# Kernel tuning notes

Measured on AMD Instinct MI355X. Metric: run time of the kernel, lower is better.

## Reference

```python
import jax, jax.numpy as jnp
import numpy as np

DIM = 768
HEADS = 12
HEAD_DIM = DIM // HEADS
EPS = 1e-6
LN_EPS = 1e-5


def setup_inputs() -> dict:
    key = jax.random.key(0)
    k1, k2, k3, k4 = jax.random.split(key, 4)
    x = jax.random.normal(k1, (8, 4096, DIM), dtype=jnp.float32)
    ln_gamma = jnp.ones((DIM,), dtype=jnp.float32)
    ln_beta = jnp.zeros((DIM,), dtype=jnp.float32)
    # torch nn.Linear weight layout: [out_features, in_features]
    w_qkv = jax.random.normal(k2, (3 * DIM, DIM), dtype=jnp.float32) * (1.0 / np.sqrt(DIM))
    w_proj = jax.random.normal(k3, (DIM, DIM), dtype=jnp.float32) * (1.0 / np.sqrt(DIM))
    b_proj = jax.random.normal(k4, (DIM,), dtype=jnp.float32) * 0.01
    return {"x": x, "ln_gamma": ln_gamma, "ln_beta": ln_beta,
            "w_qkv": w_qkv, "w_proj": w_proj, "b_proj": b_proj}


def _elu1(t):
    return jax.nn.elu(t) + 1.0


def reference(x, ln_gamma, ln_beta, w_qkv, w_proj, b_proj):
    bsz, n, dim = x.shape
    # LayerNorm
    mu = jnp.mean(x, axis=-1, keepdims=True)
    var = jnp.mean(jnp.square(x - mu), axis=-1, keepdims=True)
    y = (x - mu) * jax.lax.rsqrt(var + LN_EPS) * ln_gamma + ln_beta
    # qkv projection: [b, n, 3*dim]
    qkv = jnp.einsum('bnd,ed->bne', y, w_qkv)
    qkv = qkv.reshape(bsz, n, 3, HEADS, HEAD_DIM)
    qkv = jnp.transpose(qkv, (2, 0, 3, 1, 4))  # [3, b, h, n, hd]
    q, k, v = _elu1(qkv[0]), _elu1(qkv[1]), qkv[2]
    # kv outer-product sum over tokens: [b, h, d, e]
    kv = jnp.einsum('bhnd,bhne->bhde', k, v)
    k_sum = jnp.sum(k, axis=2)                              # [b, h, d]
    z = 1.0 / (jnp.einsum('bhnd,bhd->bhn', q, k_sum) + EPS)  # [b, h, n]
    out = jnp.einsum('bhnd,bhde->bhne', q, kv) * z[..., None]
    out = jnp.transpose(out, (0, 2, 1, 3)).reshape(bsz, n, dim)
    return jnp.einsum('bnd,ed->bne', out, w_proj) + b_proj
```

## Files before the change

### kernel.cpp

```cpp
#include <hip/hip_runtime.h>
#include <stdint.h>

typedef __bf16 bf16;
typedef __bf16 bf16x4 __attribute__((ext_vector_type(4)));
typedef __bf16 bf16x8 __attribute__((ext_vector_type(8)));
typedef float  f32x4  __attribute__((ext_vector_type(4)));

#define DIM   768
#define HEADS 12
#define HD    64
#define SEQ   4096
#define NKT2  12

__device__ __forceinline__ void gload16(const void* g, void* l) {
  typedef const __attribute__((address_space(1))) uint32_t* gp_t;
  typedef __attribute__((address_space(3))) uint32_t* lp_t;
  gp_t gp = reinterpret_cast<gp_t>(reinterpret_cast<uintptr_t>(g));
  lp_t lp = reinterpret_cast<lp_t>(reinterpret_cast<uintptr_t>(l));
  __builtin_amdgcn_global_load_lds(gp, lp, 16, 0, 0);
}

__global__ __launch_bounds__(256) void wcvt_kernel(const float* __restrict__ src,
                                                   bf16* __restrict__ dst) {
  int i = (blockIdx.x * 256 + threadIdx.x) * 4;
  float4 v = *reinterpret_cast<const float4*>(src + i);
  bf16x4 o;
  o[0] = (bf16)v.x; o[1] = (bf16)v.y; o[2] = (bf16)v.z; o[3] = (bf16)v.w;
  *reinterpret_cast<bf16x4*>(dst + i) = o;
}

__global__ __launch_bounds__(256) void ln_kernel(const float* __restrict__ x,
    const float* __restrict__ gam, const float* __restrict__ bet,
    bf16* __restrict__ y) {
  const int tid = threadIdx.x, w = tid >> 6, l = tid & 63;
  const int row = blockIdx.x * 4 + w;
  const float* xr = x + (long)row * DIM;
  float4 v[3];
  float s = 0.f, ss = 0.f;
#pragma unroll
  for (int j = 0; j < 3; j++) {
    v[j] = *reinterpret_cast<const float4*>(xr + l * 4 + j * 256);
    s  += v[j].x + v[j].y + v[j].z + v[j].w;
    ss += v[j].x * v[j].x + v[j].y * v[j].y + v[j].z * v[j].z + v[j].w * v[j].w;
  }
#pragma unroll
  for (int m = 1; m < 64; m <<= 1) { s += __shfl_xor(s, m); ss += __shfl_xor(ss, m); }
  const float mu = s * (1.f / 768.f);
  const float rstd = rsqrtf(ss * (1.f / 768.f) - mu * mu + 1e-5f);
  bf16* yr = y + (long)row * DIM;
#pragma unroll
  for (int j = 0; j < 3; j++) {
    int c = l * 4 + j * 256;
    float4 g4 = *reinterpret_cast<const float4*>(gam + c);
    float4 b4 = *reinterpret_cast<const float4*>(bet + c);
    bf16x4 o;
    o[0] = (bf16)((v[j].x - mu) * rstd * g4.x + b4.x);
    o[1] = (bf16)((v[j].y - mu) * rstd * g4.y + b4.y);
    o[2] = (bf16)((v[j].z - mu) * rstd * g4.z + b4.z);
    o[3] = (bf16)((v[j].w - mu) * rstd * g4.w + b4.w);
    *reinterpret_cast<bf16x4*>(yr + c) = o;
  }
}

template <int MODE>
__global__ __launch_bounds__(512, 4) void gemm_kernel(
    const bf16* __restrict__ A, const bf16* __restrict__ Bw,
    bf16* __restrict__ qb, bf16* __restrict__ kb, bf16* __restrict__ vb,
    float* __restrict__ outp, const float* __restrict__ bias) {
  __shared__ __align__(16) char lds[32768];
  const int tid = threadIdx.x;
  const int wid = tid >> 6, l = tid & 63;
  const int wr = wid >> 2, wc = wid & 3;
  const int l16 = l & 15, l4 = l >> 4;

  const int NT = (MODE == 0) ? 18 : 6;
  const int nwg = NT * 256;
  const int orig = blockIdx.x;
  const int wgid = (orig & 7) * (nwg >> 3) + (orig >> 3);
  const int mt = wgid / NT, nt = wgid % NT;

  const int L0 = tid * 16, L1 = 8192 + tid * 16;
  const int r0 = L0 >> 7, s0 = (L0 >> 4) & 7;
  const int r1 = L1 >> 7, s1 = (L1 >> 4) & 7;
  const bf16* pA0 = A + (long)(mt * 128 + r0) * DIM + (s0 ^ (r0 & 7)) * 8;
  const bf16* pA1 = A + (long)(mt * 128 + r1) * DIM + (s1 ^ (r1 & 7)) * 8;
  const bf16* pB0 = Bw + (long)(nt * 128 + r0) * DIM + (s0 ^ (r0 & 7)) * 8;
  const bf16* pB1 = Bw + (long)(nt * 128 + r1) * DIM + (s1 ^ (r1 & 7)) * 8;

  int offA[2][4], offB[2][2];
#pragma unroll
  for (int ks = 0; ks < 2; ks++) {
#pragma unroll
    for (int mi = 0; mi < 4; mi++) {
      int row = wr * 64 + mi * 16 + l16;
      offA[ks][mi] = row * 128 + (((l4 + 4 * ks) ^ (l16 & 7)) << 4);
    }
#pragma unroll
    for (int ni = 0; ni < 2; ni++) {
      int row = wc * 32 + ni * 16 + l16;
      offB[ks][ni] = 16384 + row * 128 + (((l4 + 4 * ks) ^ (l16 & 7)) << 4);
    }
  }

  f32x4 acc[4][2];
#pragma unroll
  for (int m = 0; m < 4; m++)
#pragma unroll
    for (int n = 0; n < 2; n++) { f32x4 z4 = {0.f, 0.f, 0.f, 0.f}; acc[m][n] = z4; }

  for (int t = 0; t < NKT2; t++) {
    __syncthreads();
    gload16(pA0 + t * 64, lds + L0);
    gload16(pA1 + t * 64, lds + L1);
    gload16(pB0 + t * 64, lds + 16384 + L0);
    gload16(pB1 + t * 64, lds + 16384 + L1);
    __syncthreads();
#pragma unroll
    for (int ks = 0; ks < 2; ks++) {
      bf16x8 a[4], b[2];
#pragma unroll
      for (int mi = 0; mi < 4; mi++)
        a[mi] = *reinterpret_cast<const bf16x8*>(lds + offA[ks][mi]);
#pragma unroll
      for (int ni = 0; ni < 2; ni++)
        b[ni] = *reinterpret_cast<const bf16x8*>(lds + offB[ks][ni]);
#pragma unroll
      for (int mi = 0; mi < 4; mi++)
#pragma unroll
        for (int ni = 0; ni < 2; ni++)
          acc[mi][ni] = __builtin_amdgcn_mfma_f32_16x16x32_bf16(a[mi], b[ni], acc[mi][ni], 0, 0, 0);
    }
  }

  if constexpr (MODE == 0) {
    const int s = nt / 6;
    const int j = nt % 6;
    if (s == 0) {
      bf16* Cs = (bf16*)lds;
      __syncthreads();
#pragma unroll
      for (int mi = 0; mi < 4; mi++)
#pragma unroll
        for (int ni = 0; ni < 2; ni++)
#pragma unroll
          for (int i = 0; i < 4; i++) {
            float val = acc[mi][ni][i];
            val = val > 0.f ? val + 1.f : __expf(val);
            Cs[(wr * 64 + mi * 16 + l4 * 4 + i) * 128 + wc * 32 + ni * 16 + l16] = (bf16)val;
          }
      __syncthreads();
#pragma unroll
      for (int it = 0; it < 4; it++) {
        int bi = it * 8192 + tid * 16;
        int row = bi >> 8;
        int col = (bi & 255) >> 1;
        int h = j * 2 + (col >> 6), d = col & 63;
        int trow = mt * 128 + row;
        int bb = trow >> 12, tok = trow & 4095;
        *reinterpret_cast<bf16x8*>(qb +
            ((long)(bb * HEADS + h) * SEQ + tok) * HD + d) =
            *reinterpret_cast<const bf16x8*>(Cs + (bi >> 1));
      }
    } else {
      bf16* dst0 = (s == 1) ? kb : vb;
      __syncthreads();
#pragma unroll
      for (int mi = 0; mi < 4; mi++)
#pragma unroll
        for (int ni = 0; ni < 2; ni++)
#pragma unroll
          for (int i = 0; i < 4; i++) {
            float val = acc[mi][ni][i];
            if (s == 1) val = val > 0.f ? val + 1.f : __expf(val);
            int tr = wr * 64 + mi * 16 + l4 * 4 + i;
            int cc = wc * 32 + ni * 16 + l16;
            *reinterpret_cast<bf16*>(lds + tr * 256 + ((cc * 2) ^ ((tr & 7) << 4))) = (bf16)val;
          }
      __syncthreads();
      const int cc = tid & 127;
      const int sp2 = tid >> 7;
      const int hh = j * 2 + (cc >> 6), dd = cc & 63;
      const int bb = (mt * 128) >> 12;
      const int n0 = ((mt * 128) & 4095) + sp2 * 32;
      bf16* dstp = dst0 + ((long)(bb * HEADS + hh) * HD + dd) * SEQ + n0;
#pragma unroll
      for (int q8i = 0; q8i < 4; q8i++) {
        bf16x8 o;
#pragma unroll
        for (int jj = 0; jj < 8; jj++) {
          int tok = sp2 * 32 + q8i * 8 + jj;
          o[jj] = *reinterpret_cast<const bf16*>(lds + tok * 256 + ((cc * 2) ^ ((tok & 7) << 4)));
        }
        *reinterpret_cast<bf16x8*>(dstp + q8i * 8) = o;
      }
    }
  } else {
#pragma unroll
    for (int ni = 0; ni < 2; ni++) {
      int col = nt * 128 + wc * 32 + ni * 16 + l16;
      float bv = bias[col];
#pragma unroll
      for (int mi = 0; mi < 4; mi++)
#pragma unroll
        for (int i = 0; i < 4; i++) {
          long trow = mt * 128 + wr * 64 + mi * 16 + l4 * 4 + i;
          outp[trow * DIM + col] = acc[mi][ni][i] + bv;
        }
    }
  }
}

__global__ __launch_bounds__(256) void kv_kernel(
    const bf16* __restrict__ ktb, const bf16* __restrict__ vtb,
    float* __restrict__ kv_part, float* __restrict__ ks_part) {
  __shared__ __align__(16) char lds[32768];
  const int head = blockIdx.x, sp = blockIdx.y;
  const int tid = threadIdx.x;
  const int wid = tid >> 6, l = tid & 63;
  const int wd = wid >> 1, we = wid & 1;
  const int l16 = l & 15, l4 = l >> 4;

  int offK[4][2], offV[4][2];
#pragma unroll
  for (int ks = 0; ks < 4; ks++) {
#pragma unroll
    for (int mi = 0; mi < 2; mi++) {
      int row = wd * 32 + mi * 16 + l16;
      offK[ks][mi] = row * 256 + ((ks * 64 + l4 * 16) ^ ((row & 7) << 4));
    }
#pragma unroll
    for (int ni = 0; ni < 2; ni++) {
      int row = we * 32 + ni * 16 + l16;
      offV[ks][ni] = 16384 + row * 256 + ((ks * 64 + l4 * 16) ^ ((row & 7) << 4));
    }
  }
  const bf16* srcK[4]; const bf16* srcV[4]; int ldst[4];
#pragma unroll
  for (int g = 0; g < 4; g++) {
    int L = g * 4096 + tid * 16;
    int r = L >> 8, cb = L & 255;
    int ce = (cb ^ ((r & 7) << 4)) >> 1;
    srcK[g] = ktb + ((long)head * HD + r) * SEQ + sp * 512 + ce;
    srcV[g] = vtb + ((long)head * HD + r) * SEQ + sp * 512 + ce;
    ldst[g] = L;
  }

  f32x4 acc[2][2];
#pragma unroll
  for (int m = 0; m < 2; m++)
#pragma unroll
    for (int n = 0; n < 2; n++) { f32x4 z4 = {0.f, 0.f, 0.f, 0.f}; acc[m][n] = z4; }
  float ksf = 0.f;
  const int ksd = tid >> 2, ksq = tid & 3;

  for (int c = 0; c < 4; c++) {
    __syncthreads();
#pragma unroll
    for (int g = 0; g < 4; g++) {
      gload16(srcK[g] + c * 128, lds + ldst[g]);
      gload16(srcV[g] + c * 128, lds + 16384 + ldst[g]);
    }
    __syncthreads();
#pragma unroll
    for (int q = 0; q < 4; q++) {
      bf16x8 k8 = *reinterpret_cast<const bf16x8*>(
          lds + ksd * 256 + ((ksq * 64 + q * 16) ^ ((ksd & 7) << 4)));
#pragma unroll
      for (int jj = 0; jj < 8; jj++) ksf += (float)k8[jj];
    }
#pragma unroll
    for (int ks = 0; ks < 4; ks++) {
      bf16x8 a[2], b[2];
      a[0] = *reinterpret_cast<const bf16x8*>(lds + offK[ks][0]);
      a[1] = *reinterpret_cast<const bf16x8*>(lds + offK[ks][1]);
      b[0] = *reinterpret_cast<const bf16x8*>(lds + offV[ks][0]);
      b[1] = *reinterpret_cast<const bf16x8*>(lds + offV[ks][1]);
#pragma unroll
      for (int mi = 0; mi < 2; mi++)
#pragma unroll
        for (int ni = 0; ni < 2; ni++)
          acc[mi][ni] = __builtin_amdgcn_mfma_f32_16x16x32_bf16(a[mi], b[ni], acc[mi][ni], 0, 0, 0);
    }
  }
  ksf += __shfl_xor(ksf, 1);
  ksf += __shfl_xor(ksf, 2);
  if (ksq == 0) ks_part[(head * 8 + sp) * 64 + ksd] = ksf;

  __syncthreads();
#pragma unroll
  for (int mi = 0; mi < 2; mi++)
#pragma unroll
    for (int ni = 0; ni < 2; ni++)
#pragma unroll
      for (int i = 0; i < 4; i++) {
        int dd = wd * 32 + mi * 16 + l4 * 4 + i;
        int ee = we * 32 + ni * 16 + l16;
        *reinterpret_cast<float*>(lds + dd * 256 + ((ee * 4) ^ ((dd & 7) << 4))) = acc[mi][ni][i];
      }
  __syncthreads();
  float* dst = kv_part + (long)(head * 8 + sp) * 4096;
  const int dd2 = tid >> 2, eq = tid & 3;
#pragma unroll
  for (int q = 0; q < 4; q++) {
    f32x4 v4 = *reinterpret_cast<const f32x4*>(
        lds + dd2 * 256 + ((eq * 64 + q * 16) ^ ((dd2 & 7) << 4)));
    *reinterpret_cast<f32x4*>(dst + dd2 * 64 + eq * 16 + q * 4) = v4;
  }
}

__global__ __launch_bounds__(256) void kvfin_kernel(const float* __restrict__ kv_part,
    const float* __restrict__ ks_part, bf16* __restrict__ kvT, float* __restrict__ ksum) {
  const int head = blockIdx.x, tid = threadIdx.x;
  const long base = (long)head * 8 * 4096;
  const int d = tid >> 2, ecol = (tid & 3) * 16;
  float s[16];
#pragma unroll
  for (int q = 0; q < 16; q++) s[q] = 0.f;
  for (int sp = 0; sp < 8; sp++) {
    const float* p = kv_part + base + sp * 4096 + d * 64 + ecol;
#pragma unroll
    for (int q = 0; q < 16; q++) s[q] += p[q];
  }
#pragma unroll
  for (int q = 0; q < 16; q++) kvT[head * 4096 + (ecol + q) * 64 + d] = (bf16)s[q];
  if (tid < 64) {
    float t = 0.f;
    for (int sp = 0; sp < 8; sp++) t += ks_part[(head * 8 + sp) * 64 + tid];
    ksum[head * 64 + tid] = t;
  }
}

__global__ __launch_bounds__(256) void qout_kernel(const bf16* __restrict__ qb,
    const bf16* __restrict__ kvT, const float* __restrict__ ksum,
    bf16* __restrict__ outp) {
  __shared__ __align__(16) bf16 Qs[128 * 64];
  __shared__ __align__(16) bf16 Bs2[64 * 64];
  __shared__ float ksum_s[64];
  __shared__ float z_s[128];
  const int head = blockIdx.x, tt = blockIdx.y;
  const int b = head / HEADS, h = head % HEADS;
  const int tid = threadIdx.x, w = tid >> 6, l = tid & 63;
  const int l16 = l & 15, l4 = l >> 4;
  const bf16* Qg = qb + (long)(head * SEQ + tt * 128) * HD;
#pragma unroll
  for (int r = 0; r < 4; r++) gload16(Qg + r * 2048 + tid * 8, Qs + r * 2048 + tid * 8);
#pragma unroll
  for (int r = 0; r < 2; r++)
    gload16(kvT + head * 4096 + r * 2048 + tid * 8, Bs2 + r * 2048 + tid * 8);
  if (tid < 64) ksum_s[tid] = ksum[head * 64 + tid];
  __syncthreads();
  {
    const int tok = tid >> 1, hf = tid & 1;
    float dsum = 0.f;
#pragma unroll
    for (int q = 0; q < 4; q++) {
      bf16x8 q8 = *reinterpret_cast<const bf16x8*>(Qs + tok * 64 + hf * 32 + q * 8);
#pragma unroll
      for (int jj = 0; jj < 8; jj++) dsum += (float)q8[jj] * ksum_s[hf * 32 + q * 8 + jj];
    }
    dsum += __shfl_xor(dsum, 1);
    if (hf == 0) z_s[tok] = 1.f / (dsum + 1e-6f);
  }
  f32x4 acc[2][4];
#pragma unroll
  for (int m = 0; m < 2; m++)
#pragma unroll
    for (int n = 0; n < 4; n++) { f32x4 z4 = {0.f, 0.f, 0.f, 0.f}; acc[m][n] = z4; }
#pragma unroll
  for (int kk = 0; kk < 2; kk++) {
    bf16x8 af[2], bfr[4];
#pragma unroll
    for (int m = 0; m < 2; m++)
      af[m] = *reinterpret_cast<const bf16x8*>(Qs + (w * 32 + m * 16 + l16) * 64 + kk * 32 + l4 * 8);
#pragma unroll
    for (int n = 0; n < 4; n++)
      bfr[n] = *reinterpret_cast<const bf16x8*>(Bs2 + (n * 16 + l16) * 64 + kk * 32 + l4 * 8);
#pragma unroll
    for (int m = 0; m < 2; m++)
#pragma unroll
      for (int n = 0; n < 4; n++)
        acc[m][n] = __builtin_amdgcn_mfma_f32_16x16x32_bf16(af[m], bfr[n], acc[m][n], 0, 0, 0);
  }
  __syncthreads();
#pragma unroll
  for (int m = 0; m < 2; m++)
#pragma unroll
    for (int n = 0; n < 4; n++)
#pragma unroll
      for (int i = 0; i < 4; i++) {
        int row = w * 32 + m * 16 + l4 * 4 + i;
        Qs[row * 64 + n * 16 + l16] = (bf16)(acc[m][n][i] * z_s[row]);
      }
  __syncthreads();
#pragma unroll
  for (int r = 0; r < 4; r++) {
    int idx = r * 2048 + tid * 8;
    int row = idx >> 6, col = idx & 63;
    *reinterpret_cast<bf16x8*>(outp + (long)(b * SEQ + tt * 128 + row) * DIM + h * HD + col) =
        *reinterpret_cast<const bf16x8*>(Qs + idx);
  }
}

extern "C" void kernel_launch(void* const* d_in, const int* in_sizes, int n_in,
                              void* d_out, int out_size, void* d_ws, size_t ws_size,
                              hipStream_t stream) {
  const float* x     = (const float*)d_in[0];
  const float* gam   = (const float*)d_in[1];
  const float* bet   = (const float*)d_in[2];
  const float* wqkv  = (const float*)d_in[3];
  const float* wproj = (const float*)d_in[4];
  const float* bproj = (const float*)d_in[5];
  float* out = (float*)d_out;
  char* ws = (char*)d_ws;

  bf16*  y       = (bf16*)(ws);
  bf16*  qb      = (bf16*)(ws + 50331648);
  bf16*  kb      = (bf16*)(ws + 100663296);
  bf16*  vb      = (bf16*)(ws + 150994944);
  bf16*  wqkv_b  = (bf16*)(ws + 201326592);
  bf16*  wproj_b = (bf16*)(ws + 204865536);
  float* kv_part = (float*)(ws + 206045184);
  float* ks_part = (float*)(ws + 218628096);
  bf16*  kvT     = (bf16*)(ws + 218824704);
  float* ksum    = (float*)(ws + 219611136);

  wcvt_kernel<<<1728, 256, 0, stream>>>(wqkv, wqkv_b);
  wcvt_kernel<<<576, 256, 0, stream>>>(wproj, wproj_b);
  ln_kernel<<<8192, 256, 0, stream>>>(x, gam, bet, y);
  gemm_kernel<0><<<dim3(18 * 256), 512, 0, stream>>>(y, wqkv_b, qb, kb, vb, nullptr, nullptr);
  kv_kernel<<<dim3(96, 8), 256, 0, stream>>>(kb, vb, kv_part, ks_part);
  kvfin_kernel<<<96, 256, 0, stream>>>(kv_part, ks_part, kvT, ksum);
  qout_kernel<<<dim3(96, 32), 256, 0, stream>>>(qb, kvT, ksum, y);
  gemm_kernel<1><<<dim3(6 * 256), 512, 0, stream>>>(y, wproj_b, nullptr, nullptr, nullptr, out, bproj);
}
```

Baseline: 269.8 us.

## Enlarge GEMM tile to 256x128 with 4x4 MFMA per wave, direct K/V stores

The GEMM block tile grows from 128x128 to 256x128, and each wave now computes a 64x64 sub-tile with a 4x4 grid of MFMA accumulators. This raises arithmetic intensity per LDS load and halves the grid size. The K/V epilogue drops the LDS transpose and writes bf16x4 token-contiguous vectors straight to global memory. The Q epilogue is staged in two halves through LDS. The two weight-conversion launches are merged into one. The costs are higher register pressure (64 accumulator floats) and 48KB of LDS per block, which may limit occupancy under the (512,4) launch bounds, plus narrower global stores for K/V.

```diff
diff --git a/kernel.cpp b/kernel.cpp
--- a/kernel.cpp
+++ b/kernel.cpp
@@ -20,13 +20,17 @@
   __builtin_amdgcn_global_load_lds(gp, lp, 16, 0, 0);
 }
 
-__global__ __launch_bounds__(256) void wcvt_kernel(const float* __restrict__ src,
-                                                   bf16* __restrict__ dst) {
-  int i = (blockIdx.x * 256 + threadIdx.x) * 4;
-  float4 v = *reinterpret_cast<const float4*>(src + i);
+__global__ __launch_bounds__(256) void wcvt_kernel(const float* __restrict__ wq,
+    const float* __restrict__ wp, bf16* __restrict__ dq, bf16* __restrict__ dp) {
+  long i = (long)(blockIdx.x * 256 + threadIdx.x) * 4;
+  const long NQ = 3L * DIM * DIM;
+  const float* src; bf16* dst; long off;
+  if (i < NQ) { src = wq; dst = dq; off = i; }
+  else        { src = wp; dst = dp; off = i - NQ; }
+  float4 v = *reinterpret_cast<const float4*>(src + off);
   bf16x4 o;
   o[0] = (bf16)v.x; o[1] = (bf16)v.y; o[2] = (bf16)v.z; o[3] = (bf16)v.w;
-  *reinterpret_cast<bf16x4*>(dst + i) = o;
+  *reinterpret_cast<bf16x4*>(dst + off) = o;
 }
 
 __global__ __launch_bounds__(256) void ln_kernel(const float* __restrict__ x,
@@ -67,67 +71,75 @@
     const bf16* __restrict__ A, const bf16* __restrict__ Bw,
     bf16* __restrict__ qb, bf16* __restrict__ kb, bf16* __restrict__ vb,
     float* __restrict__ outp, const float* __restrict__ bias) {
-  __shared__ __align__(16) char lds[32768];
+  __shared__ __align__(16) char lds[49152];
   const int tid = threadIdx.x;
   const int wid = tid >> 6, l = tid & 63;
-  const int wr = wid >> 2, wc = wid & 3;
+  const int wr = wid >> 1, wc = wid & 1;
   const int l16 = l & 15, l4 = l >> 4;
 
   const int NT = (MODE == 0) ? 18 : 6;
-  const int nwg = NT * 256;
+  const int nwg = NT * 128;
   const int orig = blockIdx.x;
   const int wgid = (orig & 7) * (nwg >> 3) + (orig >> 3);
   const int mt = wgid / NT, nt = wgid % NT;
 
-  const int L0 = tid * 16, L1 = 8192 + tid * 16;
-  const int r0 = L0 >> 7, s0 = (L0 >> 4) & 7;
-  const int r1 = L1 >> 7, s1 = (L1 >> 4) & 7;
-  const bf16* pA0 = A + (long)(mt * 128 + r0) * DIM + (s0 ^ (r0 & 7)) * 8;
-  const bf16* pA1 = A + (long)(mt * 128 + r1) * DIM + (s1 ^ (r1 & 7)) * 8;
-  const bf16* pB0 = Bw + (long)(nt * 128 + r0) * DIM + (s0 ^ (r0 & 7)) * 8;
-  const bf16* pB1 = Bw + (long)(nt * 128 + r1) * DIM + (s1 ^ (r1 & 7)) * 8;
-
-  int offA[2][4], offB[2][2];
+  const bf16* pA[4]; const bf16* pB[2]; int lA[4], lB[2];
+#pragma unroll
+  for (int g = 0; g < 4; g++) {
+    int L = g * 8192 + tid * 16;
+    int r = L >> 7, sl = (L >> 4) & 7;
+    pA[g] = A + (long)(mt * 256 + r) * DIM + (sl ^ (r & 7)) * 8;
+    lA[g] = L;
+  }
+#pragma unroll
+  for (int g = 0; g < 2; g++) {
+    int L = g * 8192 + tid * 16;
+    int r = L >> 7, sl = (L >> 4) & 7;
+    pB[g] = Bw + (long)(nt * 128 + r) * DIM + (sl ^ (r & 7)) * 8;
+    lB[g] = 32768 + L;
+  }
+
+  int offA[2][4], offB[2][4];
 #pragma unroll
   for (int ks = 0; ks < 2; ks++) {
 #pragma unroll
     for (int mi = 0; mi < 4; mi++) {
       int row = wr * 64 + mi * 16 + l16;
-      offA[ks][mi] = row * 128 + (((l4 + 4 * ks) ^ (l16 & 7)) << 4);
-    }
-#pragma unroll
-    for (int ni = 0; ni < 2; ni++) {
-      int row = wc * 32 + ni * 16 + l16;
-      offB[ks][ni] = 16384 + row * 128 + (((l4 + 4 * ks) ^ (l16 & 7)) << 4);
-    }
-  }
-
-  f32x4 acc[4][2];
+      offA[ks][mi] = row * 128 + (((l4 + 4 * ks) ^ (row & 7)) << 4);
+    }
+#pragma unroll
+    for (int ni = 0; ni < 4; ni++) {
+      int row = wc * 64 + ni * 16 + l16;
+      offB[ks][ni] = 32768 + row * 128 + (((l4 + 4 * ks) ^ (row & 7)) << 4);
+    }
+  }
+
+  f32x4 acc[4][4];
 #pragma unroll
   for (int m = 0; m < 4; m++)
 #pragma unroll
-    for (int n = 0; n < 2; n++) { f32x4 z4 = {0.f, 0.f, 0.f, 0.f}; acc[m][n] = z4; }
+    for (int n = 0; n < 4; n++) { f32x4 z4 = {0.f, 0.f, 0.f, 0.f}; acc[m][n] = z4; }
 
   for (int t = 0; t < NKT2; t++) {
     __syncthreads();
-    gload16(pA0 + t * 64, lds + L0);
-    gload16(pA1 + t * 64, lds + L1);
-    gload16(pB0 + t * 64, lds + 16384 + L0);
-    gload16(pB1 + t * 64, lds + 16384 + L1);
+#pragma unroll
+    for (int g = 0; g < 4; g++) gload16(pA[g] + t * 64, lds + lA[g]);
+#pragma unroll
+    for (int g = 0; g < 2; g++) gload16(pB[g] + t * 64, lds + lB[g]);
     __syncthreads();
 #pragma unroll
     for (int ks = 0; ks < 2; ks++) {
-      bf16x8 a[4], b[2];
+      bf16x8 a[4], b[4];
 #pragma unroll
       for (int mi = 0; mi < 4; mi++)
         a[mi] = *reinterpret_cast<const bf16x8*>(lds + offA[ks][mi]);
 #pragma unroll
-      for (int ni = 0; ni < 2; ni++)
+      for (int ni = 0; ni < 4; ni++)
         b[ni] = *reinterpret_cast<const bf16x8*>(lds + offB[ks][ni]);
 #pragma unroll
       for (int mi = 0; mi < 4; mi++)
 #pragma unroll
-        for (int ni = 0; ni < 2; ni++)
+        for (int ni = 0; ni < 4; ni++)
           acc[mi][ni] = __builtin_amdgcn_mfma_f32_16x16x32_bf16(a[mi], b[ni], acc[mi][ni], 0, 0, 0);
     }
   }
@@ -137,73 +149,69 @@
     const int j = nt % 6;
     if (s == 0) {
       bf16* Cs = (bf16*)lds;
-      __syncthreads();
-#pragma unroll
-      for (int mi = 0; mi < 4; mi++)
-#pragma unroll
-        for (int ni = 0; ni < 2; ni++)
-#pragma unroll
-          for (int i = 0; i < 4; i++) {
-            float val = acc[mi][ni][i];
-            val = val > 0.f ? val + 1.f : __expf(val);
-            Cs[(wr * 64 + mi * 16 + l4 * 4 + i) * 128 + wc * 32 + ni * 16 + l16] = (bf16)val;
-          }
-      __syncthreads();
-#pragma unroll
-      for (int it = 0; it < 4; it++) {
-        int bi = it * 8192 + tid * 16;
-        int row = bi >> 8;
-        int col = (bi & 255) >> 1;
-        int h = j * 2 + (col >> 6), d = col & 63;
-        int trow = mt * 128 + row;
-        int bb = trow >> 12, tok = trow & 4095;
-        *reinterpret_cast<bf16x8*>(qb +
-            ((long)(bb * HEADS + h) * SEQ + tok) * HD + d) =
-            *reinterpret_cast<const bf16x8*>(Cs + (bi >> 1));
+#pragma unroll
+      for (int pr = 0; pr < 2; pr++) {
+        __syncthreads();
+        if ((wr >> 1) == pr) {
+#pragma unroll
+          for (int mi = 0; mi < 4; mi++)
+#pragma unroll
+            for (int ni = 0; ni < 4; ni++)
+#pragma unroll
+              for (int i = 0; i < 4; i++) {
+                float val = acc[mi][ni][i];
+                val = val > 0.f ? val + 1.f : __expf(val);
+                int row = (wr & 1) * 64 + mi * 16 + l4 * 4 + i;
+                int col = wc * 64 + ni * 16 + l16;
+                Cs[row * 128 + col] = (bf16)val;
+              }
+        }
+        __syncthreads();
+#pragma unroll
+        for (int it = 0; it < 4; it++) {
+          int bi = it * 8192 + tid * 16;
+          int row = bi >> 8;
+          int col = (bi & 255) >> 1;
+          int h = j * 2 + (col >> 6), d = col & 63;
+          int trow = mt * 256 + pr * 128 + row;
+          int bb = trow >> 12, tok = trow & 4095;
+          *reinterpret_cast<bf16x8*>(qb +
+              ((long)(bb * HEADS + h) * SEQ + tok) * HD + d) =
+              *reinterpret_cast<const bf16x8*>(Cs + (bi >> 1));
+        }
       }
     } else {
       bf16* dst0 = (s == 1) ? kb : vb;
-      __syncthreads();
+      const int bb = (mt * 256) >> 12;
+      const int tokbase = (mt * 256) & 4095;
 #pragma unroll
       for (int mi = 0; mi < 4; mi++)
 #pragma unroll
-        for (int ni = 0; ni < 2; ni++)
+        for (int ni = 0; ni < 4; ni++) {
+          int col = wc * 64 + ni * 16 + l16;
+          int h = j * 2 + (col >> 6), d = col & 63;
+          int tok = tokbase + wr * 64 + mi * 16 + l4 * 4;
+          bf16x4 o;
 #pragma unroll
           for (int i = 0; i < 4; i++) {
             float val = acc[mi][ni][i];
             if (s == 1) val = val > 0.f ? val + 1.f : __expf(val);
-            int tr = wr * 64 + mi * 16 + l4 * 4 + i;
-            int cc = wc * 32 + ni * 16 + l16;
-            *reinterpret_cast<bf16*>(lds + tr * 256 + ((cc * 2) ^ ((tr & 7) << 4))) = (bf16)val;
+            o[i] = (bf16)val;
           }
-      __syncthreads();
-      const int cc = tid & 127;
-      const int sp2 = tid >> 7;
-      const int hh = j * 2 + (cc >> 6), dd = cc & 63;
-      const int bb = (mt * 128) >> 12;
-      const int n0 = ((mt * 128) & 4095) + sp2 * 32;
-      bf16* dstp = dst0 + ((long)(bb * HEADS + hh) * HD + dd) * SEQ + n0;
-#pragma unroll
-      for (int q8i = 0; q8i < 4; q8i++) {
-        bf16x8 o;
-#pragma unroll
-        for (int jj = 0; jj < 8; jj++) {
-          int tok = sp2 * 32 + q8i * 8 + jj;
-          o[jj] = *reinterpret_cast<const bf16*>(lds + tok * 256 + ((cc * 2) ^ ((tok & 7) << 4)));
+          *reinterpret_cast<bf16x4*>(dst0 +
+              ((long)(bb * HEADS + h) * HD + d) * SEQ + tok) = o;
         }
-        *reinterpret_cast<bf16x8*>(dstp + q8i * 8) = o;
-      }
     }
   } else {
 #pragma unroll
-    for (int ni = 0; ni < 2; ni++) {
-      int col = nt * 128 + wc * 32 + ni * 16 + l16;
+    for (int ni = 0; ni < 4; ni++) {
+      int col = nt * 128 + wc * 64 + ni * 16 + l16;
       float bv = bias[col];
 #pragma unroll
       for (int mi = 0; mi < 4; mi++)
 #pragma unroll
         for (int i = 0; i < 4; i++) {
-          long trow = mt * 128 + wr * 64 + mi * 16 + l4 * 4 + i;
+          long trow = mt * 256 + wr * 64 + mi * 16 + l4 * 4 + i;
           outp[trow * DIM + col] = acc[mi][ni][i] + bv;
         }
     }
@@ -424,12 +432,11 @@
   bf16*  kvT     = (bf16*)(ws + 218824704);
   float* ksum    = (float*)(ws + 219611136);
 
-  wcvt_kernel<<<1728, 256, 0, stream>>>(wqkv, wqkv_b);
-  wcvt_kernel<<<576, 256, 0, stream>>>(wproj, wproj_b);
+  wcvt_kernel<<<2304, 256, 0, stream>>>(wqkv, wproj, wqkv_b, wproj_b);
   ln_kernel<<<8192, 256, 0, stream>>>(x, gam, bet, y);
-  gemm_kernel<0><<<dim3(18 * 256), 512, 0, stream>>>(y, wqkv_b, qb, kb, vb, nullptr, nullptr);
+  gemm_kernel<0><<<dim3(18 * 128), 512, 0, stream>>>(y, wqkv_b, qb, kb, vb, nullptr, nullptr);
   kv_kernel<<<dim3(96, 8), 256, 0, stream>>>(kb, vb, kv_part, ks_part);
   kvfin_kernel<<<96, 256, 0, stream>>>(kv_part, ks_part, kvT, ksum);
   qout_kernel<<<dim3(96, 32), 256, 0, stream>>>(qb, kvT, ksum, y);
-  gemm_kernel<1><<<dim3(6 * 256), 512, 0, stream>>>(y, wproj_b, nullptr, nullptr, nullptr, out, bproj);
-}
+  gemm_kernel<1><<<dim3(6 * 128), 512, 0, stream>>>(y, wproj_b, nullptr, nullptr, nullptr, out, bproj);
+}
```

Measured after the change: 313.4 us. 16.1% more time.

## Vectorize K/V transpose epilogue, fix swizzle index, merge weight conversions

Applied to the files above, without the earlier changes.

The K/V epilogue of the QKV GEMM now writes each lane's four accumulator values as one bf16x4 into a column-major (feature-by-token) LDS tile. Each thread then reads contiguous bf16x8 token runs for the transposed global store, replacing 32 scalar LDS reads per thread. The operand LDS read offsets now XOR with the row index instead of the lane index, which is identical since the row offsets are multiples of 8. The two weight-conversion launches are merged into one kernel launch. The new LDS write pattern may cause bank conflicts.

```diff
diff --git a/kernel.cpp b/kernel.cpp
--- a/kernel.cpp
+++ b/kernel.cpp
@@ -20,13 +20,17 @@
   __builtin_amdgcn_global_load_lds(gp, lp, 16, 0, 0);
 }
 
-__global__ __launch_bounds__(256) void wcvt_kernel(const float* __restrict__ src,
-                                                   bf16* __restrict__ dst) {
-  int i = (blockIdx.x * 256 + threadIdx.x) * 4;
-  float4 v = *reinterpret_cast<const float4*>(src + i);
+__global__ __launch_bounds__(256) void wcvt_kernel(const float* __restrict__ wq,
+    const float* __restrict__ wp, bf16* __restrict__ dq, bf16* __restrict__ dp) {
+  long i = (long)(blockIdx.x * 256 + threadIdx.x) * 4;
+  const long NQ = 3L * DIM * DIM;
+  const float* src; bf16* dst; long off;
+  if (i < NQ) { src = wq; dst = dq; off = i; }
+  else        { src = wp; dst = dp; off = i - NQ; }
+  float4 v = *reinterpret_cast<const float4*>(src + off);
   bf16x4 o;
   o[0] = (bf16)v.x; o[1] = (bf16)v.y; o[2] = (bf16)v.z; o[3] = (bf16)v.w;
-  *reinterpret_cast<bf16x4*>(dst + i) = o;
+  *reinterpret_cast<bf16x4*>(dst + off) = o;
 }
 
 __global__ __launch_bounds__(256) void ln_kernel(const float* __restrict__ x,
@@ -93,12 +97,12 @@
 #pragma unroll
     for (int mi = 0; mi < 4; mi++) {
       int row = wr * 64 + mi * 16 + l16;
-      offA[ks][mi] = row * 128 + (((l4 + 4 * ks) ^ (l16 & 7)) << 4);
+      offA[ks][mi] = row * 128 + (((l4 + 4 * ks) ^ (row & 7)) << 4);
     }
 #pragma unroll
     for (int ni = 0; ni < 2; ni++) {
       int row = wc * 32 + ni * 16 + l16;
-      offB[ks][ni] = 16384 + row * 128 + (((l4 + 4 * ks) ^ (l16 & 7)) << 4);
+      offB[ks][ni] = 16384 + row * 128 + (((l4 + 4 * ks) ^ (row & 7)) << 4);
     }
   }
 
@@ -167,31 +171,30 @@
 #pragma unroll
       for (int mi = 0; mi < 4; mi++)
 #pragma unroll
-        for (int ni = 0; ni < 2; ni++)
+        for (int ni = 0; ni < 2; ni++) {
+          int col = wc * 32 + ni * 16 + l16;
+          int tok0 = wr * 64 + mi * 16 + l4 * 4;
+          bf16x4 o;
 #pragma unroll
           for (int i = 0; i < 4; i++) {
             float val = acc[mi][ni][i];
             if (s == 1) val = val > 0.f ? val + 1.f : __expf(val);
-            int tr = wr * 64 + mi * 16 + l4 * 4 + i;
-            int cc = wc * 32 + ni * 16 + l16;
-            *reinterpret_cast<bf16*>(lds + tr * 256 + ((cc * 2) ^ ((tr & 7) << 4))) = (bf16)val;
+            o[i] = (bf16)val;
           }
+          *reinterpret_cast<bf16x4*>(lds + col * 256 + ((tok0 * 2) ^ ((col & 7) << 4))) = o;
+        }
       __syncthreads();
-      const int cc = tid & 127;
-      const int sp2 = tid >> 7;
-      const int hh = j * 2 + (cc >> 6), dd = cc & 63;
       const int bb = (mt * 128) >> 12;
-      const int n0 = ((mt * 128) & 4095) + sp2 * 32;
-      bf16* dstp = dst0 + ((long)(bb * HEADS + hh) * HD + dd) * SEQ + n0;
-#pragma unroll
-      for (int q8i = 0; q8i < 4; q8i++) {
-        bf16x8 o;
-#pragma unroll
-        for (int jj = 0; jj < 8; jj++) {
-          int tok = sp2 * 32 + q8i * 8 + jj;
-          o[jj] = *reinterpret_cast<const bf16*>(lds + tok * 256 + ((cc * 2) ^ ((tok & 7) << 4)));
-        }
-        *reinterpret_cast<bf16x8*>(dstp + q8i * 8) = o;
+      const int tokbase = (mt * 128) & 4095;
+#pragma unroll
+      for (int p = 0; p < 4; p++) {
+        int col = p * 32 + (tid >> 4);
+        int tok = (tid & 15) * 8;
+        int h = j * 2 + (col >> 6), d = col & 63;
+        bf16x8 o8 = *reinterpret_cast<const bf16x8*>(
+            lds + col * 256 + ((tok * 2) ^ ((col & 7) << 4)));
+        *reinterpret_cast<bf16x8*>(dst0 +
+            ((long)(bb * HEADS + h) * HD + d) * SEQ + tokbase + tok) = o8;
       }
     }
   } else {
@@ -424,8 +427,7 @@
   bf16*  kvT     = (bf16*)(ws + 218824704);
   float* ksum    = (float*)(ws + 219611136);
 
-  wcvt_kernel<<<1728, 256, 0, stream>>>(wqkv, wqkv_b);
-  wcvt_kernel<<<576, 256, 0, stream>>>(wproj, wproj_b);
+  wcvt_kernel<<<2304, 256, 0, stream>>>(wqkv, wproj, wqkv_b, wproj_b);
   ln_kernel<<<8192, 256, 0, stream>>>(x, gam, bet, y);
   gemm_kernel<0><<<dim3(18 * 256), 512, 0, stream>>>(y, wqkv_b, qb, kb, vb, nullptr, nullptr);
   kv_kernel<<<dim3(96, 8), 256, 0, stream>>>(kb, vb, kv_part, ks_part);
```

Result: faster. 254.9 us (-5.5%).
